# Kernel tuning notes

Measured on AMD Instinct MI355X. Metric: run time of the kernel, lower is better.

The kernel has to match this reference:

```python
import jax, jax.numpy as jnp
import numpy as np

B, S, D, H, KD, HID = 8, 1024, 512, 8, 64, 32


def setup_inputs() -> dict:
    key = jax.random.key(0)
    ks = jax.random.split(key, 13)
    s = 0.05
    return {
        "src": jax.random.normal(ks[0], (B, S, D), jnp.float32),
        "Wq": jax.random.normal(ks[1], (H, KD, D), jnp.float32) * s,
        "Wk": jax.random.normal(ks[2], (H, KD, D), jnp.float32) * s,
        "Wv": jax.random.normal(ks[3], (H, KD, D), jnp.float32) * s,
        "c_raw": jnp.ones((H,), jnp.float32),              # nn.Parameter(1.0) per head
        "L": jnp.full((H,), 2.0, jnp.float32),             # nn.Parameter(2.0) per head
        "w1": jax.random.normal(ks[4], (H, HID), jnp.float32) * s,   # Linear(1,HID) weight
        "b1": jax.random.normal(ks[5], (H, HID), jnp.float32) * s,
        "W2": jax.random.normal(ks[6], (H, HID, HID), jnp.float32) * s,  # [out,in]
        "b2": jax.random.normal(ks[7], (H, HID), jnp.float32) * s,
        "w3": jax.random.normal(ks[8], (H, HID), jnp.float32) * s,   # Linear(HID,1) weight
        "b3": jax.random.normal(ks[9], (H,), jnp.float32) * s,
        "Wo": jax.random.normal(ks[10], (D, D), jnp.float32) * s,
    }


def _gelu(x):
    return jax.nn.gelu(x, approximate=False)  # torch nn.GELU default (erf)


def reference(src, Wq, Wk, Wv, c_raw, L, w1, b1, W2, b2, w3, b3, Wo):
    Bc, Sc, Dc = src.shape
    Hh, Kd = Wq.shape[0], Wq.shape[1]
    # ---- FIRE bias: raw[i,j] = log1p(c*(i-j)) / log1p(c*max(L, i+1)) for j<i else 0
    ii = jnp.arange(Sc, dtype=jnp.float32)[:, None]   # [S,1]
    jj = jnp.arange(Sc, dtype=jnp.float32)[None, :]   # [1,S]
    d = ii - jj                                       # [S,S]
    c = jax.nn.softplus(c_raw)[:, None, None]         # [H,1,1]
    num = jnp.log1p(c * jnp.where(d > 0, d, 1.0)[None])          # safe for d<=0
    den = jnp.log1p(c * jnp.maximum(L[:, None, None], ii[None] + 1.0))
    raw = jnp.where(d[None] > 0, num / den, 0.0)      # [H,S,S]
    # ---- f_theta MLP applied elementwise (Linear(1,h)->GELU->Linear(h,h)->GELU->Linear(h,1))
    h1 = _gelu(raw[..., None] * w1[:, None, None, :] + b1[:, None, None, :])   # [H,S,S,HID]
    h2 = _gelu(jnp.einsum('hijk,hlk->hijl', h1, W2) + b2[:, None, None, :])    # [H,S,S,HID]
    bias = jnp.einsum('hijk,hk->hij', h2, w3) + b3[:, None, None]              # [H,S,S]
    # ---- causal mask (strict upper triangle -> -inf)
    causal = jnp.arange(Sc)[None, :] > jnp.arange(Sc)[:, None]
    bias = jnp.where(causal[None], -jnp.inf, bias)
    # ---- attention per head
    q = jnp.einsum('bsd,hkd->bhsk', src, Wq)
    k = jnp.einsum('bsd,hkd->bhsk', src, Wk)
    v = jnp.einsum('bsd,hkd->bhsk', src, Wv)
    logits = jnp.einsum('bhik,bhjk->bhij', q, k) / jnp.sqrt(jnp.float32(Kd)) + bias[None]
    attn = jax.nn.softmax(logits, axis=-1)
    o = jnp.einsum('bhij,bhjk->bhik', attn, v)        # [B,H,S,KD]
    o = jnp.transpose(o, (0, 2, 1, 3)).reshape(Bc, Sc, Hh * Kd)  # concat heads
    return o @ Wo.T
```

## Files before the change

### kernel.cpp

```cpp
#include <hip/hip_runtime.h>
#include <math.h>

#define S_LEN 1024
#define NHEAD 8
#define BATCH 8
#define KDIM  64
#define HID   32
#define NT    2048
#define LOG2E 1.4426950408889634f
#define TRI(q) ((q) * ((q) + 1) / 2)
#define PERM(m) (((m) & 0x20) | (((m) & 0x0C) << 1) | (((m) & 0x10) >> 2) | ((m) & 3))
#define SWZ(row) (((((row) >> 3) & 1) << 2) | ((row) & 3))

typedef __attribute__((ext_vector_type(8))) short bf16x8;
typedef __attribute__((ext_vector_type(4))) float f32x4;
typedef unsigned short ushort_t;

__device__ inline ushort_t f2bf(float f) {
  union { float f; unsigned u; } v; v.f = f;
  unsigned u = v.u;
  return (ushort_t)((u + 0x7FFFu + ((u >> 16) & 1u)) >> 16);
}
__device__ inline float bf2f(ushort_t u) {
  union { unsigned x; float f; } v; v.x = ((unsigned)u) << 16; return v.f;
}
__device__ inline unsigned cvtpk_bf16(float lo, float hi) {
  unsigned r;
  asm("v_cvt_pk_bf16_f32 %0, %1, %2" : "=v"(r) : "v"(lo), "v"(hi));
  return r;
}

__device__ inline void gl_lds16(const ushort_t* g, ushort_t* l) {
  __builtin_amdgcn_global_load_lds(
      (const __attribute__((address_space(1))) unsigned int*)g,
      (__attribute__((address_space(3))) unsigned int*)l, 16, 0, 0);
}

__global__ __launch_bounds__(256) void prep(
    const float* __restrict__ s, const float* __restrict__ wq,
    const float* __restrict__ wk, const float* __restrict__ wv,
    const float* __restrict__ wo,
    ushort_t* __restrict__ sb, ushort_t* __restrict__ wqb,
    ushort_t* __restrict__ wkb, ushort_t* __restrict__ wvb,
    ushort_t* __restrict__ wob,
    const float* __restrict__ c_raw, const float* __restrict__ Lp,
    const float* __restrict__ w1, const float* __restrict__ b1,
    const float* __restrict__ W2, const float* __restrict__ b2,
    const float* __restrict__ w3, const float* __restrict__ b3,
    float* __restrict__ num_g, float* __restrict__ rden_g,
    float* __restrict__ gtab_g) {
  __shared__ float h1s[8][33];
  const int bx = blockIdx.x;
  const int tid = threadIdx.x;
  if (bx < 5120) {
    const float* src; ushort_t* dst; int base; float scale = 1.0f;
    if (bx < 4096)      { src = s;  dst = sb;  base = bx; }
    else if (bx < 4352) { src = wq; dst = wqb; base = bx - 4096; scale = 0.125f * LOG2E; }
    else if (bx < 4608) { src = wk; dst = wkb; base = bx - 4352; }
    else if (bx < 4864) { src = wv; dst = wvb; base = bx - 4608; }
    else                { src = wo; dst = wob; base = bx - 4864; }
    const int i = (base * 256 + tid) * 4;
    float4 v = *(const float4*)&src[i];
    ushort4 o;
    o.x = f2bf(v.x * scale); o.y = f2bf(v.y * scale);
    o.z = f2bf(v.z * scale); o.w = f2bf(v.w * scale);
    *(ushort4*)&dst[i] = o;
  } else {
    const int idx = bx - 5120;
    const int h = idx / 257;
    const int xb = idx % 257;
    const float cr = c_raw[h];
    const float c = (cr > 20.f) ? cr : log1pf(expf(cr));
    const int gid = xb * 256 + tid;
    if (gid < S_LEN) {
      num_g[h * S_LEN + gid] = log1pf(c * (float)gid);
      rden_g[h * S_LEN + gid] = 1.0f / log1pf(c * fmaxf(Lp[h], (float)(gid + 1)));
    }
    const int pl = tid >> 5;
    const int j = tid & 31;
    const int pt = xb * 8 + pl;
    const float x = (float)pt * (1.0f / NT);
    float v = x * w1[h * HID + j] + b1[h * HID + j];
    h1s[pl][j] = 0.5f * v * (1.0f + erff(v * 0.70710678118f));
    __syncthreads();
    float sm = b2[h * HID + j];
    const float* w2r = W2 + ((size_t)(h * HID + j)) * HID;
    #pragma unroll
    for (int k = 0; k < HID; ++k) sm += w2r[k] * h1s[pl][k];
    float g = 0.5f * sm * (1.0f + erff(sm * 0.70710678118f));
    float y = w3[h * HID + j] * g;
    #pragma unroll
    for (int off = 1; off < 32; off <<= 1) y += __shfl_xor(y, off);
    if (j == 0 && pt <= NT) gtab_g[h * (NT + 1) + pt] = (y + b3[h]) * LOG2E;
  }
}

__device__ __forceinline__ void qkv_tile(
    ushort_t* sAB, const ushort_t* __restrict__ A,
    const ushort_t* __restrict__ Wq_, const ushort_t* __restrict__ Wk_,
    const ushort_t* __restrict__ Wv_,
    ushort_t* __restrict__ Qo, ushort_t* __restrict__ Ko,
    ushort_t* __restrict__ Vto, int m0, int n0, int tid) {
  ushort_t* sA = sAB;
  ushort_t* sW = sAB + 4096;
  const int lane = tid & 63, w = tid >> 6, quad = lane >> 4, l16 = lane & 15;
  f32x4 acc[3][4];
  #pragma unroll
  for (int z = 0; z < 3; ++z)
    #pragma unroll
    for (int nb = 0; nb < 4; ++nb) acc[z][nb] = (f32x4)0.0f;

  const int r8 = lane >> 3;
  const int gc = (lane & 7) ^ r8;
  const int sw = l16 & 7;
  const ushort_t* Wz[3] = {Wq_, Wk_, Wv_};

  for (int kt = 0; kt < 512; kt += 64) {
    __syncthreads();
    #pragma unroll
    for (int j = 0; j < 2; ++j) {
      const int row = w * 16 + j * 8 + r8;
      gl_lds16(&A[(size_t)(m0 + row) * 512 + kt + gc * 8], &sA[(w * 16 + j * 8) * 64]);
      #pragma unroll
      for (int z = 0; z < 3; ++z)
        gl_lds16(&Wz[z][(size_t)(n0 + row) * 512 + kt + gc * 8],
                 &sW[z * 4096 + (w * 16 + j * 8) * 64]);
    }
    __syncthreads();
    #pragma unroll
    for (int ks = 0; ks < 2; ++ks) {
      const int off = ((ks * 4 + quad) ^ sw) * 8;
      bf16x8 af = *(const bf16x8*)&sA[(w * 16 + l16) * 64 + off];
      #pragma unroll
      for (int z = 0; z < 3; ++z)
        #pragma unroll
        for (int nb = 0; nb < 4; ++nb) {
          bf16x8 wf = *(const bf16x8*)&sW[z * 4096 + (nb * 16 + l16) * 64 + off];
          acc[z][nb] = __builtin_amdgcn_mfma_f32_16x16x32_bf16(af, wf, acc[z][nb], 0, 0, 0);
        }
    }
  }

  const int bb = m0 >> 10, sbase = m0 & 1023;
  #pragma unroll
  for (int z = 0; z < 2; ++z) {
    ushort_t* outp = z ? Ko : Qo;
    #pragma unroll
    for (int nb = 0; nb < 4; ++nb)
      #pragma unroll
      for (int r = 0; r < 4; ++r) {
        int m = m0 + w * 16 + quad * 4 + r;
        int n = n0 + nb * 16 + l16;
        int ss = m & 1023, hh = n >> 6, kd = n & 63;
        outp[(((size_t)(bb * NHEAD + hh)) * S_LEN + ss) * KDIM + kd] = f2bf(acc[z][nb][r]);
      }
  }
  __syncthreads();
  #pragma unroll
  for (int nb = 0; nb < 4; ++nb)
    #pragma unroll
    for (int r = 0; r < 4; ++r) {
      int nl = nb * 16 + l16;
      int ml = w * 16 + quad * 4 + r;
      sAB[nl * 64 + (((ml >> 3) ^ (nl & 7)) * 8) + (ml & 7)] = f2bf(acc[2][nb][r]);
    }
  __syncthreads();
  const int nl = tid >> 2, seg = tid & 3;
  const int ng = n0 + nl, hh = ng >> 6, kd = ng & 63;
  ushort_t* vout = Vto + (((size_t)(bb * NHEAD + hh)) * KDIM + kd) * S_LEN;
  #pragma unroll
  for (int c2 = 0; c2 < 2; ++c2) {
    int mc = seg * 2 + c2;
    bf16x8 vr = *(bf16x8*)&sAB[nl * 64 + ((mc ^ (nl & 7)) * 8)];
    *(bf16x8*)&vout[sbase + mc * 8] = vr;
  }
}

__device__ __forceinline__ void gemm_tile(
    ushort_t* sAB, const ushort_t* __restrict__ A, const ushort_t* __restrict__ Wp,
    float* __restrict__ outp, int m0, int n0, int tid) {
  ushort_t* sA = sAB;
  ushort_t* sB = sAB + 4096;
  const int lane = tid & 63, w = tid >> 6, quad = lane >> 4, l16 = lane & 15;
  f32x4 acc[4];
  #pragma unroll
  for (int nb = 0; nb < 4; ++nb) acc[nb] = (f32x4)0.0f;

  const int r8 = lane >> 3;
  const int gc = (lane & 7) ^ r8;
  const int sw = l16 & 7;

  for (int kt = 0; kt < 512; kt += 64) {
    __syncthreads();
    #pragma unroll
    for (int j = 0; j < 2; ++j) {
      const int row = w * 16 + j * 8 + r8;
      gl_lds16(&A[(size_t)(m0 + row) * 512 + kt + gc * 8], &sA[(w * 16 + j * 8) * 64]);
      gl_lds16(&Wp[(size_t)(n0 + row) * 512 + kt + gc * 8], &sB[(w * 16 + j * 8) * 64]);
    }
    __syncthreads();
    #pragma unroll
    for (int ks = 0; ks < 2; ++ks) {
      const int off = ((ks * 4 + quad) ^ sw) * 8;
      bf16x8 af = *(bf16x8*)&sA[(w * 16 + l16) * 64 + off];
      #pragma unroll
      for (int nb = 0; nb < 4; ++nb) {
        bf16x8 bfr = *(bf16x8*)&sB[(nb * 16 + l16) * 64 + off];
        acc[nb] = __builtin_amdgcn_mfma_f32_16x16x32_bf16(af, bfr, acc[nb], 0, 0, 0);
      }
    }
  }
  #pragma unroll
  for (int nb = 0; nb < 4; ++nb) {
    #pragma unroll
    for (int r = 0; r < 4; ++r) {
      int m = m0 + w * 16 + quad * 4 + r;
      int n = n0 + nb * 16 + l16;
      outp[(size_t)m * 512 + n] = acc[nb][r];
    }
  }
}

__global__ __launch_bounds__(256) void gemm_bias(
    const ushort_t* __restrict__ A,
    const ushort_t* __restrict__ W0, const ushort_t* __restrict__ W1,
    const ushort_t* __restrict__ W2w,
    void* __restrict__ out0, void* __restrict__ out1, void* __restrict__ out2,
    int scatter, int nGemm,
    const float* __restrict__ num_g, const float* __restrict__ rden_g,
    const float* __restrict__ gtab_g, ushort_t* __restrict__ biaspre) {
  __shared__ __align__(16) ushort_t sAB[16384];
  const int tid = threadIdx.x;
  if ((int)blockIdx.x < nGemm) {
    const int tile = blockIdx.x;
    const int m0 = (tile & 127) * 64;
    const int n0 = (tile >> 7) * 64;
    if (scatter) {
      qkv_tile(sAB, A, W0, W1, W2w, (ushort_t*)out0, (ushort_t*)out1,
               (ushort_t*)out2, m0, n0, tid);
    } else {
      gemm_tile(sAB, A, W0, (float*)out0, m0, n0, tid);
    }
  } else {
    const int idx = blockIdx.x - nGemm;
    const int h = idx / 68;
    const int pair = idx % 68;
    float* gtab_s = (float*)sAB;
    float* num_s = gtab_s + 2052;
    float* rden_s = num_s + 1024;
    for (int i = tid; i <= NT; i += 256) gtab_s[i] = gtab_g[h * (NT + 1) + i];
    for (int i = tid; i < S_LEN; i += 256) num_s[i] = num_g[h * S_LEN + i];
    const int sub = tid >> 7, tid2 = tid & 127;
    const int tileIdx = pair * 2 + sub;
    int qt = 0;
    while (TRI(qt + 1) <= tileIdx) ++qt;
    const int t = tileIdx - TRI(qt);
    if (tid2 < 64) rden_s[sub * 64 + tid2] = rden_g[h * S_LEN + qt * 64 + tid2];
    __syncthreads();
    const int w = tid2 >> 6, lane = tid2 & 63, quad = lane >> 4, l16 = lane & 15;
    ushort_t vals[32];
    #pragma unroll
    for (int qg = 0; qg < 2; ++qg) {
      const int iloc = w * 32 + qg * 16 + l16;
      const int i = qt * 64 + iloc;
      const float rden = rden_s[sub * 64 + iloc];
      #pragma unroll
      for (int nb = 0; nb < 4; ++nb)
        #pragma unroll
        for (int r = 0; r < 4; ++r) {
          const int m = nb * 16 + quad * 4 + r;
          const int j = t * 64 + PERM(m);
          ushort_t out;
          if (j > i) {
            out = 0xFF80;
          } else {
            const int d = i - j;
            float x = num_s[d] * rden;
            float tf = x * (float)NT;
            int it = (int)tf; it = it < (NT - 1) ? it : (NT - 1);
            float fr = tf - (float)it;
            float ga = gtab_s[it];
            out = f2bf(ga + (gtab_s[it + 1] - ga) * fr);
          }
          vals[qg * 16 + nb * 4 + r] = out;
        }
    }
    ushort_t* dst = &biaspre[((size_t)(h * 136 + tileIdx) * 128 + tid2) * 32];
    uint4 u[2];
    #pragma unroll
    for (int half = 0; half < 2; ++half) {
      #pragma unroll
      for (int v = 0; v < 8; ++v) ((ushort_t*)&u[0])[v] = vals[half * 16 + v];
      #pragma unroll
      for (int v = 0; v < 8; ++v) ((ushort_t*)&u[1])[v] = vals[half * 16 + 8 + v];
      *(uint4*)(dst + half * 16) = u[0];
      *(uint4*)(dst + half * 16 + 8) = u[1];
    }
  }
}

__global__ __launch_bounds__(256) void fire_attn_mfma(
    const ushort_t* __restrict__ Qg, const ushort_t* __restrict__ Kg,
    const ushort_t* __restrict__ Vtg, const ushort_t* __restrict__ biaspre,
    ushort_t* __restrict__ Ob) {
  __shared__ __align__(16) ushort_t sKV[16384];
  const int tid = threadIdx.x;
  const int lane = tid & 63, w = tid >> 6;
  const int pair = w >> 1, wq = w & 1;
  const int quad = lane >> 4, l16 = lane & 15;
  const int g = blockIdx.x >> 6;
  const int qt = (g < 8) ? (15 - g) : (g - 8);
  const int bh = blockIdx.x & 63, h = bh & 7, b = bh >> 3;
  const int tid2 = wq * 64 + lane;

  bf16x8 q[2][2];
  {
    const size_t qb = (size_t)bh * S_LEN + qt * 64 + wq * 32;
    #pragma unroll
    for (int qg = 0; qg < 2; ++qg)
      #pragma unroll
      for (int ks = 0; ks < 2; ++ks)
        q[qg][ks] = *(const bf16x8*)&Qg[(qb + qg * 16 + l16) * KDIM + ks * 32 + quad * 8];
  }

  const size_t kb = (size_t)bh * S_LEN * KDIM;
  const ushort_t* bptr = &biaspre[((size_t)(h * 136 + TRI(qt)) * 128 + tid2) * 32];
  const int srow8 = lane >> 3;
  const int sc = lane & 7;

  ushort_t* Kp = sKV + pair * 4096;
  ushort_t* Vp = sKV + 8192 + pair * 4096;

  auto stageKV = [&](int t) {
    #pragma unroll
    for (int j = 0; j < 4; ++j) {
      const int row = (wq * 4 + j) * 8 + srow8;
      const int cc = sc ^ SWZ(row);
      gl_lds16(&Kg[kb + (size_t)(t * 64 + row) * 64 + cc * 8], &Kp[(wq * 4 + j) * 512]);
      gl_lds16(&Vtg[kb + (size_t)row * 1024 + t * 64 + cc * 8], &Vp[(wq * 4 + j) * 512]);
    }
  };

  f32x4 o[2][4];
  float ll[2] = {0.f, 0.f};
  #pragma unroll
  for (int qg = 0; qg < 2; ++qg)
    #pragma unroll
    for (int nb = 0; nb < 4; ++nb) o[qg][nb] = (f32x4)0.0f;

  const int hA = (qt + 2) >> 1;
  for (int it = 0; it < hA; ++it) {
    const int t = pair ? (hA + it) : it;
    const bool act = (!pair) || (t <= qt);
    if (act) stageKV(t);
    __syncthreads();
    if (act) {
      uint4 bb0 = ((const uint4*)(bptr + (size_t)t * 4096))[0];
      uint4 bb1 = ((const uint4*)(bptr + (size_t)t * 4096))[1];
      uint4 bb2 = ((const uint4*)(bptr + (size_t)t * 4096))[2];
      uint4 bb3 = ((const uint4*)(bptr + (size_t)t * 4096))[3];

      f32x4 s[2][4];
      #pragma unroll
      for (int qg = 0; qg < 2; ++qg)
        #pragma unroll
        for (int nb = 0; nb < 4; ++nb) s[qg][nb] = (f32x4)0.0f;
      #pragma unroll
      for (int ks = 0; ks < 2; ++ks) {
        #pragma unroll
        for (int nb = 0; nb < 4; ++nb) {
          const int rk = PERM(nb * 16 + l16);
          bf16x8 ak = *(const bf16x8*)&Kp[rk * 64 + (((ks * 4 + quad) ^ SWZ(rk)) * 8)];
          #pragma unroll
          for (int qg = 0; qg < 2; ++qg)
            s[qg][nb] = __builtin_amdgcn_mfma_f32_16x16x32_bf16(ak, q[qg][ks], s[qg][nb], 0, 0, 0);
        }
      }

      unsigned pk[2][4][2];
      #pragma unroll
      for (int qg = 0; qg < 2; ++qg) {
        #pragma unroll
        for (int nb = 0; nb < 4; ++nb) {
          const int v = qg * 16 + nb * 4;
          const uint4& bq = (v < 8) ? bb0 : (v < 16) ? bb1 : (v < 24) ? bb2 : bb3;
          const ushort_t* bu = (const ushort_t*)&bq;
          float p0 = __builtin_amdgcn_exp2f(s[qg][nb][0] + bf2f(bu[(v + 0) & 7]));
          float p1 = __builtin_amdgcn_exp2f(s[qg][nb][1] + bf2f(bu[(v + 1) & 7]));
          float p2 = __builtin_amdgcn_exp2f(s[qg][nb][2] + bf2f(bu[(v + 2) & 7]));
          float p3 = __builtin_amdgcn_exp2f(s[qg][nb][3] + bf2f(bu[(v + 3) & 7]));
          ll[qg] += (p0 + p1) + (p2 + p3);
          pk[qg][nb][0] = cvtpk_bf16(p0, p1);
          pk[qg][nb][1] = cvtpk_bf16(p2, p3);
        }
      }

      #pragma unroll
      for (int ks = 0; ks < 2; ++ks) {
        bf16x8 pf[2];
        #pragma unroll
        for (int qg = 0; qg < 2; ++qg) {
          union { bf16x8 v; unsigned u[4]; } pkx;
          pkx.u[0] = pk[qg][2 * ks][0];
          pkx.u[1] = pk[qg][2 * ks][1];
          pkx.u[2] = pk[qg][2 * ks + 1][0];
          pkx.u[3] = pk[qg][2 * ks + 1][1];
          pf[qg] = pkx.v;
        }
        #pragma unroll
        for (int nb = 0; nb < 4; ++nb) {
          const int rv = nb * 16 + l16;
          bf16x8 av = *(const bf16x8*)&Vp[rv * 64 + (((ks * 4 + quad) ^ SWZ(rv)) * 8)];
          #pragma unroll
          for (int qg = 0; qg < 2; ++qg)
            o[qg][nb] = __builtin_amdgcn_mfma_f32_16x16x32_bf16(av, pf[qg], o[qg][nb], 0, 0, 0);
        }
      }
    }
    __syncthreads();
  }

  float* cb = (float*)sKV;
  if (pair == 1) {
    float* my = cb + tid2 * 34;
    #pragma unroll
    for (int qg = 0; qg < 2; ++qg)
      #pragma unroll
      for (int nb = 0; nb < 4; ++nb)
        #pragma unroll
        for (int r = 0; r < 4; ++r) my[qg * 16 + nb * 4 + r] = o[qg][nb][r];
    my[32] = ll[0]; my[33] = ll[1];
  }
  __syncthreads();
  if (pair == 0) {
    const float* pb = cb + tid2 * 34;
    #pragma unroll
    for (int qg = 0; qg < 2; ++qg)
      #pragma unroll
      for (int nb = 0; nb < 4; ++nb)
        #pragma unroll
        for (int r = 0; r < 4; ++r) o[qg][nb][r] += pb[qg * 16 + nb * 4 + r];
    ll[0] += pb[32]; ll[1] += pb[33];

    #pragma unroll
    for (int qg = 0; qg < 2; ++qg) {
      float rs = ll[qg];
      rs += __shfl_xor(rs, 16);
      rs += __shfl_xor(rs, 32);
      const float rl = 1.0f / rs;
      const size_t ob = ((size_t)(b * S_LEN + qt * 64 + wq * 32 + qg * 16 + l16)) * 512 + h * KDIM;
      #pragma unroll
      for (int nb = 0; nb < 4; ++nb) {
        ushort4 ov;
        ov.x = f2bf(o[qg][nb][0] * rl);
        ov.y = f2bf(o[qg][nb][1] * rl);
        ov.z = f2bf(o[qg][nb][2] * rl);
        ov.w = f2bf(o[qg][nb][3] * rl);
        *(ushort4*)&Ob[ob + nb * 16 + quad * 4] = ov;
      }
    }
  }
}

extern "C" void kernel_launch(void* const* d_in, const int* in_sizes, int n_in,
                              void* d_out, int out_size, void* d_ws, size_t ws_size,
                              hipStream_t stream) {
  const float* src   = (const float*)d_in[0];
  const float* Wq    = (const float*)d_in[1];
  const float* Wk    = (const float*)d_in[2];
  const float* Wv    = (const float*)d_in[3];
  const float* c_raw = (const float*)d_in[4];
  const float* Lp    = (const float*)d_in[5];
  const float* w1    = (const float*)d_in[6];
  const float* b1    = (const float*)d_in[7];
  const float* W2    = (const float*)d_in[8];
  const float* b2    = (const float*)d_in[9];
  const float* w3    = (const float*)d_in[10];
  const float* b3    = (const float*)d_in[11];
  const float* Wo    = (const float*)d_in[12];
  float* outp = (float*)d_out;

  const size_t SRC_E = 4194304;
  const size_t W_E   = 262144;
  const size_t QKV_E = 4194304;
  ushort_t* srcb = (ushort_t*)d_ws;
  ushort_t* Wqb  = srcb + SRC_E;
  ushort_t* Wkb  = Wqb + W_E;
  ushort_t* Wvb  = Wkb + W_E;
  ushort_t* Wob  = Wvb + W_E;
  ushort_t* Qb   = Wob + W_E;
  ushort_t* Kb   = Qb + QKV_E;
  ushort_t* Vtb  = Kb + QKV_E;
  ushort_t* Obb  = Vtb + QKV_E;
  ushort_t* biaspre = Obb + QKV_E;
  float* numb  = (float*)(biaspre + (size_t)NHEAD * 136 * 128 * 32);
  float* rdenb = numb + NHEAD * S_LEN;
  float* gtabb = rdenb + NHEAD * S_LEN;

  hipLaunchKernelGGL(prep, dim3(7176), dim3(256), 0, stream,
                     src, Wq, Wk, Wv, Wo, srcb, Wqb, Wkb, Wvb, Wob,
                     c_raw, Lp, w1, b1, W2, b2, w3, b3, numb, rdenb, gtabb);
  hipLaunchKernelGGL(gemm_bias, dim3(1568), dim3(256), 0, stream,
                     srcb, Wqb, Wkb, Wvb, (void*)Qb, (void*)Kb, (void*)Vtb,
                     1, 1024, numb, rdenb, gtabb, biaspre);
  hipLaunchKernelGGL(fire_attn_mfma, dim3(1024), dim3(256), 0, stream,
                     Qb, Kb, Vtb, biaspre, Obb);
  hipLaunchKernelGGL(gemm_bias, dim3(1024), dim3(256), 0, stream,
                     Obb, Wob, Wob, Wob, (void*)outp, (void*)outp, (void*)outp,
                     0, 1024, numb, rdenb, gtabb, biaspre);
}
```

Baseline: 156.5 us.

## Enlarge GEMM M-tile to 128 rows with two MFMA row blocks per wave

Both the QKV projection and the output projection GEMMs now use 128x64 tiles instead of 64x64. Each wave computes two 16-row blocks, so every loaded weight fragment feeds two MFMAs and weight traffic per output is halved. Grid sizes are halved to match, and the V-transpose staging in shared memory is widened to 128 columns. The cost is more accumulator registers, a larger LDS footprint and fewer blocks, which may lower occupancy and parallelism.

New measurement: 164.9 us. 1.05x slower.

```diff
diff --git a/kernel.cpp b/kernel.cpp
--- a/kernel.cpp
+++ b/kernel.cpp
@@ -102,13 +102,15 @@
     ushort_t* __restrict__ Qo, ushort_t* __restrict__ Ko,
     ushort_t* __restrict__ Vto, int m0, int n0, int tid) {
   ushort_t* sA = sAB;
-  ushort_t* sW = sAB + 4096;
+  ushort_t* sW = sAB + 8192;
   const int lane = tid & 63, w = tid >> 6, quad = lane >> 4, l16 = lane & 15;
-  f32x4 acc[3][4];
+  f32x4 acc[3][2][4];
   #pragma unroll
   for (int z = 0; z < 3; ++z)
     #pragma unroll
-    for (int nb = 0; nb < 4; ++nb) acc[z][nb] = (f32x4)0.0f;
+    for (int mi = 0; mi < 2; ++mi)
+      #pragma unroll
+      for (int nb = 0; nb < 4; ++nb) acc[z][mi][nb] = (f32x4)0.0f;
 
   const int r8 = lane >> 3;
   const int gc = (lane & 7) ^ r8;
@@ -118,25 +120,34 @@
   for (int kt = 0; kt < 512; kt += 64) {
     __syncthreads();
     #pragma unroll
-    for (int j = 0; j < 2; ++j) {
-      const int row = w * 16 + j * 8 + r8;
-      gl_lds16(&A[(size_t)(m0 + row) * 512 + kt + gc * 8], &sA[(w * 16 + j * 8) * 64]);
-      #pragma unroll
-      for (int z = 0; z < 3; ++z)
+    for (int j = 0; j < 4; ++j) {
+      const int row = w * 32 + j * 8 + r8;
+      gl_lds16(&A[(size_t)(m0 + row) * 512 + kt + gc * 8], &sA[(w * 32 + j * 8) * 64]);
+    }
+    #pragma unroll
+    for (int z = 0; z < 3; ++z)
+      #pragma unroll
+      for (int j = 0; j < 2; ++j) {
+        const int row = w * 16 + j * 8 + r8;
         gl_lds16(&Wz[z][(size_t)(n0 + row) * 512 + kt + gc * 8],
                  &sW[z * 4096 + (w * 16 + j * 8) * 64]);
-    }
+      }
     __syncthreads();
     #pragma unroll
     for (int ks = 0; ks < 2; ++ks) {
       const int off = ((ks * 4 + quad) ^ sw) * 8;
-      bf16x8 af = *(const bf16x8*)&sA[(w * 16 + l16) * 64 + off];
+      bf16x8 af[2];
+      #pragma unroll
+      for (int mi = 0; mi < 2; ++mi)
+        af[mi] = *(const bf16x8*)&sA[(w * 32 + mi * 16 + l16) * 64 + off];
       #pragma unroll
       for (int z = 0; z < 3; ++z)
         #pragma unroll
         for (int nb = 0; nb < 4; ++nb) {
           bf16x8 wf = *(const bf16x8*)&sW[z * 4096 + (nb * 16 + l16) * 64 + off];
-          acc[z][nb] = __builtin_amdgcn_mfma_f32_16x16x32_bf16(af, wf, acc[z][nb], 0, 0, 0);
+          #pragma unroll
+          for (int mi = 0; mi < 2; ++mi)
+            acc[z][mi][nb] = __builtin_amdgcn_mfma_f32_16x16x32_bf16(af[mi], wf, acc[z][mi][nb], 0, 0, 0);
         }
     }
   }
@@ -146,32 +157,36 @@
   for (int z = 0; z < 2; ++z) {
     ushort_t* outp = z ? Ko : Qo;
     #pragma unroll
+    for (int mi = 0; mi < 2; ++mi)
+      #pragma unroll
+      for (int nb = 0; nb < 4; ++nb)
+        #pragma unroll
+        for (int r = 0; r < 4; ++r) {
+          int m = m0 + w * 32 + mi * 16 + quad * 4 + r;
+          int n = n0 + nb * 16 + l16;
+          int ss = m & 1023, hh = n >> 6, kd = n & 63;
+          outp[(((size_t)(bb * NHEAD + hh)) * S_LEN + ss) * KDIM + kd] = f2bf(acc[z][mi][nb][r]);
+        }
+  }
+  __syncthreads();
+  #pragma unroll
+  for (int mi = 0; mi < 2; ++mi)
+    #pragma unroll
     for (int nb = 0; nb < 4; ++nb)
       #pragma unroll
       for (int r = 0; r < 4; ++r) {
-        int m = m0 + w * 16 + quad * 4 + r;
-        int n = n0 + nb * 16 + l16;
-        int ss = m & 1023, hh = n >> 6, kd = n & 63;
-        outp[(((size_t)(bb * NHEAD + hh)) * S_LEN + ss) * KDIM + kd] = f2bf(acc[z][nb][r]);
-      }
-  }
-  __syncthreads();
-  #pragma unroll
-  for (int nb = 0; nb < 4; ++nb)
-    #pragma unroll
-    for (int r = 0; r < 4; ++r) {
-      int nl = nb * 16 + l16;
-      int ml = w * 16 + quad * 4 + r;
-      sAB[nl * 64 + (((ml >> 3) ^ (nl & 7)) * 8) + (ml & 7)] = f2bf(acc[2][nb][r]);
-    }
+        int nl = nb * 16 + l16;
+        int ml = w * 32 + mi * 16 + quad * 4 + r;
+        sAB[nl * 128 + (((ml >> 3) ^ (nl & 7)) * 8) + (ml & 7)] = f2bf(acc[2][mi][nb][r]);
+      }
   __syncthreads();
   const int nl = tid >> 2, seg = tid & 3;
   const int ng = n0 + nl, hh = ng >> 6, kd = ng & 63;
   ushort_t* vout = Vto + (((size_t)(bb * NHEAD + hh)) * KDIM + kd) * S_LEN;
   #pragma unroll
-  for (int c2 = 0; c2 < 2; ++c2) {
-    int mc = seg * 2 + c2;
-    bf16x8 vr = *(bf16x8*)&sAB[nl * 64 + ((mc ^ (nl & 7)) * 8)];
+  for (int c2 = 0; c2 < 4; ++c2) {
+    int mc = seg * 4 + c2;
+    bf16x8 vr = *(bf16x8*)&sAB[nl * 128 + ((mc ^ (nl & 7)) * 8)];
     *(bf16x8*)&vout[sbase + mc * 8] = vr;
   }
 }
@@ -180,11 +195,13 @@
     ushort_t* sAB, const ushort_t* __restrict__ A, const ushort_t* __restrict__ Wp,
     float* __restrict__ outp, int m0, int n0, int tid) {
   ushort_t* sA = sAB;
-  ushort_t* sB = sAB + 4096;
+  ushort_t* sB = sAB + 8192;
   const int lane = tid & 63, w = tid >> 6, quad = lane >> 4, l16 = lane & 15;
-  f32x4 acc[4];
-  #pragma unroll
-  for (int nb = 0; nb < 4; ++nb) acc[nb] = (f32x4)0.0f;
+  f32x4 acc[2][4];
+  #pragma unroll
+  for (int mi = 0; mi < 2; ++mi)
+    #pragma unroll
+    for (int nb = 0; nb < 4; ++nb) acc[mi][nb] = (f32x4)0.0f;
 
   const int r8 = lane >> 3;
   const int gc = (lane & 7) ^ r8;
@@ -193,32 +210,42 @@
   for (int kt = 0; kt < 512; kt += 64) {
     __syncthreads();
     #pragma unroll
+    for (int j = 0; j < 4; ++j) {
+      const int row = w * 32 + j * 8 + r8;
+      gl_lds16(&A[(size_t)(m0 + row) * 512 + kt + gc * 8], &sA[(w * 32 + j * 8) * 64]);
+    }
+    #pragma unroll
     for (int j = 0; j < 2; ++j) {
       const int row = w * 16 + j * 8 + r8;
-      gl_lds16(&A[(size_t)(m0 + row) * 512 + kt + gc * 8], &sA[(w * 16 + j * 8) * 64]);
       gl_lds16(&Wp[(size_t)(n0 + row) * 512 + kt + gc * 8], &sB[(w * 16 + j * 8) * 64]);
     }
     __syncthreads();
     #pragma unroll
     for (int ks = 0; ks < 2; ++ks) {
       const int off = ((ks * 4 + quad) ^ sw) * 8;
-      bf16x8 af = *(bf16x8*)&sA[(w * 16 + l16) * 64 + off];
+      bf16x8 af[2];
+      #pragma unroll
+      for (int mi = 0; mi < 2; ++mi)
+        af[mi] = *(const bf16x8*)&sA[(w * 32 + mi * 16 + l16) * 64 + off];
       #pragma unroll
       for (int nb = 0; nb < 4; ++nb) {
-        bf16x8 bfr = *(bf16x8*)&sB[(nb * 16 + l16) * 64 + off];
-        acc[nb] = __builtin_amdgcn_mfma_f32_16x16x32_bf16(af, bfr, acc[nb], 0, 0, 0);
-      }
-    }
-  }
-  #pragma unroll
-  for (int nb = 0; nb < 4; ++nb) {
-    #pragma unroll
-    for (int r = 0; r < 4; ++r) {
-      int m = m0 + w * 16 + quad * 4 + r;
-      int n = n0 + nb * 16 + l16;
-      outp[(size_t)m * 512 + n] = acc[nb][r];
-    }
-  }
+        bf16x8 bfr = *(const bf16x8*)&sB[(nb * 16 + l16) * 64 + off];
+        #pragma unroll
+        for (int mi = 0; mi < 2; ++mi)
+          acc[mi][nb] = __builtin_amdgcn_mfma_f32_16x16x32_bf16(af[mi], bfr, acc[mi][nb], 0, 0, 0);
+      }
+    }
+  }
+  #pragma unroll
+  for (int mi = 0; mi < 2; ++mi)
+    #pragma unroll
+    for (int nb = 0; nb < 4; ++nb)
+      #pragma unroll
+      for (int r = 0; r < 4; ++r) {
+        int m = m0 + w * 32 + mi * 16 + quad * 4 + r;
+        int n = n0 + nb * 16 + l16;
+        outp[(size_t)m * 512 + n] = acc[mi][nb][r];
+      }
 }
 
 __global__ __launch_bounds__(256) void gemm_bias(
@@ -229,12 +256,12 @@
     int scatter, int nGemm,
     const float* __restrict__ num_g, const float* __restrict__ rden_g,
     const float* __restrict__ gtab_g, ushort_t* __restrict__ biaspre) {
-  __shared__ __align__(16) ushort_t sAB[16384];
+  __shared__ __align__(16) ushort_t sAB[20480];
   const int tid = threadIdx.x;
   if ((int)blockIdx.x < nGemm) {
     const int tile = blockIdx.x;
-    const int m0 = (tile & 127) * 64;
-    const int n0 = (tile >> 7) * 64;
+    const int m0 = (tile & 63) * 128;
+    const int n0 = (tile >> 6) * 64;
     if (scatter) {
       qkv_tile(sAB, A, W0, W1, W2w, (ushort_t*)out0, (ushort_t*)out1,
                (ushort_t*)out2, m0, n0, tid);
@@ -500,12 +527,12 @@
   hipLaunchKernelGGL(prep, dim3(7176), dim3(256), 0, stream,
                      src, Wq, Wk, Wv, Wo, srcb, Wqb, Wkb, Wvb, Wob,
                      c_raw, Lp, w1, b1, W2, b2, w3, b3, numb, rdenb, gtabb);
-  hipLaunchKernelGGL(gemm_bias, dim3(1568), dim3(256), 0, stream,
+  hipLaunchKernelGGL(gemm_bias, dim3(1056), dim3(256), 0, stream,
                      srcb, Wqb, Wkb, Wvb, (void*)Qb, (void*)Kb, (void*)Vtb,
-                     1, 1024, numb, rdenb, gtabb, biaspre);
+                     1, 512, numb, rdenb, gtabb, biaspre);
   hipLaunchKernelGGL(fire_attn_mfma, dim3(1024), dim3(256), 0, stream,
                      Qb, Kb, Vtb, biaspre, Obb);
-  hipLaunchKernelGGL(gemm_bias, dim3(1024), dim3(256), 0, stream,
+  hipLaunchKernelGGL(gemm_bias, dim3(512), dim3(256), 0, stream,
                      Obb, Wob, Wob, Wob, (void*)outp, (void*)outp, (void*)outp,
-                     0, 1024, numb, rdenb, gtabb, biaspre);
-}
+                     0, 512, numb, rdenb, gtabb, biaspre);
+}
```
